# Kernel tuning notes

Measured on AMD Instinct MI355X. Metric: run time of the kernel, lower is better.

The kernel has to match this reference:

```python
import jax, jax.numpy as jnp
import numpy as np

BS, X_RW, H = 16384, 768, 256  # batch, x + R*W, hidden
D_IN = X_RW + 2 * H            # 1280 = x + R*W + 2*h


def setup_inputs() -> dict:
    key = jax.random.key(0)
    ks = jax.random.split(key, 13)
    scale = 1.0 / np.sqrt(D_IN)  # nn.Linear default init range
    def lin(kw, kb):
        w = jax.random.uniform(kw, (D_IN, H), jnp.float32, -scale, scale)
        b = jax.random.uniform(kb, (H,), jnp.float32, -scale, scale)
        return w, b
    Wi, bi = lin(ks[0], ks[1])
    Wf, bf = lin(ks[2], ks[3])
    Wo, bo = lin(ks[4], ks[5])
    Ws, bs_ = lin(ks[6], ks[7])
    return {
        "input_x": jax.random.normal(ks[8], (BS, X_RW), jnp.float32),
        "previous_time": jax.random.normal(ks[9], (BS, H), jnp.float32),
        "previous_layer": jax.random.normal(ks[10], (BS, H), jnp.float32),
        "old_state": jax.random.normal(ks[11], (BS, H), jnp.float32),
        "Wi": Wi, "bi": bi, "Wf": Wf, "bf": bf,
        "Wo": Wo, "bo": bo, "Ws": Ws, "bs_": bs_,
    }


def reference(input_x, previous_time, previous_layer, old_state,
              Wi, bi, Wf, bf, Wo, bo, Ws, bs_):
    # concat once, fuse the four gate GEMMs into one [D_IN, 4H] GEMM
    s = jnp.concatenate([input_x, previous_time, previous_layer], axis=1)  # [bs, D_IN]
    W4 = jnp.concatenate([Wi, Wf, Wo, Ws], axis=1)   # [D_IN, 4H]
    b4 = jnp.concatenate([bi, bf, bo, bs_], axis=0)  # [4H]
    g = s @ W4 + b4                                   # [bs, 4H]
    i_g, f_g, o_g, c_g = jnp.split(g, 4, axis=1)
    input_gate = jax.nn.sigmoid(i_g)
    forget_gate = jax.nn.sigmoid(f_g)
    output_gate = jax.nn.sigmoid(o_g)
    new_state = forget_gate * old_state + input_gate * jnp.tanh(c_g)
    new_hidden = output_gate * jnp.tanh(new_state)
    return (new_hidden, new_state)
```

## Files before the change

kernel.cpp:

```cpp
#include <hip/hip_runtime.h>
#include <stdint.h>

#define BS   16384
#define XRW  768
#define HD   256
#define DIN  1280
#define N4   1024
#define NKT  20

typedef __attribute__((ext_vector_type(4))) float f32x4;
typedef __attribute__((ext_vector_type(8))) short s16x8;
typedef __attribute__((ext_vector_type(4))) unsigned int u32x4;

__device__ __forceinline__ unsigned short f2bf(float f) {
  uint32_t u = __builtin_bit_cast(uint32_t, f);
  u += 0x7FFFu + ((u >> 16) & 1u);
  return (unsigned short)(u >> 16);
}
__device__ __forceinline__ uint32_t cvtpk(float a, float b) {
  uint32_t d;
  asm("v_cvt_pk_bf16_f32 %0, %1, %2" : "=v"(d) : "v"(a), "v"(b));
  return d;
}
__device__ __forceinline__ float sigmoidf_(float x) {
  return 1.0f / (1.0f + __expf(-x));
}
__device__ __forceinline__ float tanhf_(float x) {
  return 1.0f - 2.0f / (__expf(2.0f * x) + 1.0f);
}
__device__ __forceinline__ void gload16(const void* g, void* l) {
  __builtin_amdgcn_global_load_lds((const __attribute__((address_space(1))) void*)g,
                                   (__attribute__((address_space(3))) void*)l, 16, 0, 0);
}

__global__ void conv_w_kernel(const float* __restrict__ Wi,
                              const float* __restrict__ Wf,
                              const float* __restrict__ Wo,
                              const float* __restrict__ Ws,
                              unsigned short* __restrict__ Wt) {
  const int np = blockIdx.x;
  const int g = (np >> 4) & 3;
  const int h = ((np >> 6) << 4) + (np & 15);
  const float* W = (g == 0) ? Wi : (g == 1) ? Wf : (g == 2) ? Wo : Ws;
  for (int k = threadIdx.x; k < DIN; k += 256)
    Wt[np * DIN + k] = f2bf(W[k * HD + h]);
}

__global__ __launch_bounds__(512, 2)
void lstm_gemm_kernel(const float* __restrict__ X,
                      const float* __restrict__ PT,
                      const float* __restrict__ PL,
                      const unsigned short* __restrict__ Wt,
                      const float* __restrict__ BI,
                      const float* __restrict__ BF,
                      const float* __restrict__ BO,
                      const float* __restrict__ BSv,
                      const float* __restrict__ OLD,
                      float* __restrict__ out) {
  __shared__ unsigned char smem[131072];
  const int tid  = threadIdx.x;
  const int wid  = tid >> 6;
  const int lane = tid & 63;

  const int H = blockIdx.x;
  const int xcd = H & 7, slot = H >> 3;
  const int mt = xcd * 8 + (slot >> 2);
  const int nt = slot & 3;
  const int wr = wid >> 2, wc = wid & 3;

  const int r8   = lane >> 3;
  const int scol = ((lane & 7) ^ r8) << 4;
  const char* gB = (const char*)Wt + (size_t)(nt * 256 + wid * 8 + r8) * (DIN * 2) + scol;

#define STAGE_B(t1, oB) do {                                                  \
    const int kb_ = (t1) * 128;                                               \
    _Pragma("unroll")                                                         \
    for (int c_ = 0; c_ < 4; ++c_)                                            \
      gload16(gB + (size_t)c_ * (64 * DIN * 2) + kb_,                         \
              &smem[65536 + (oB) + c_ * 8192 + wid * 1024]);                  \
  } while (0)

  const int arow  = tid >> 3;
  const int a7    = tid & 7;
  const int awcol = ((a7 ^ (arow & 7)) << 4);

#define ALOAD(t1, h, R0, R1, R2, R3) do {                                     \
    const float* asrc_; int astr_, aoff_;                                     \
    if ((t1) < 12)      { asrc_ = X;  astr_ = XRW; aoff_ = (t1) * 64; }       \
    else if ((t1) < 16) { asrc_ = PT; astr_ = HD;  aoff_ = ((t1) - 12) * 64; }\
    else                { asrc_ = PL; astr_ = HD;  aoff_ = ((t1) - 16) * 64; }\
    const float* ga_ = asrc_ + (size_t)(mt * 256 + arow + (h) * 128) * astr_  \
                             + aoff_ + a7 * 8;                                \
    R0 = *(const f32x4*)(ga_);                                                \
    R1 = *(const f32x4*)(ga_ + 4);                                            \
    R2 = *(const f32x4*)(ga_ + (size_t)64 * astr_);                           \
    R3 = *(const f32x4*)(ga_ + (size_t)64 * astr_ + 4);                       \
  } while (0)

#define AWRITE(oB, h, R0, R1, R2, R3) do {                                    \
    u32x4 w0_, w1_;                                                           \
    w0_.x = cvtpk(R0.x, R0.y); w0_.y = cvtpk(R0.z, R0.w);                     \
    w0_.z = cvtpk(R1.x, R1.y); w0_.w = cvtpk(R1.z, R1.w);                     \
    w1_.x = cvtpk(R2.x, R2.y); w1_.y = cvtpk(R2.z, R2.w);                     \
    w1_.z = cvtpk(R3.x, R3.y); w1_.w = cvtpk(R3.z, R3.w);                     \
    *(u32x4*)(&smem[(oB) + ((arow + (h) * 128)      << 7) + awcol]) = w0_;    \
    *(u32x4*)(&smem[(oB) + ((arow + (h) * 128 + 64) << 7) + awcol]) = w1_;    \
  } while (0)

  const int rx   = lane & 15;
  const int axor = (lane & 7) << 4;
  const int col0 = (((lane >> 4) << 4)) ^ axor;
  const int col1 = (64 + ((lane >> 4) << 4)) ^ axor;
  const int aRow = (wr * 128 + rx) * 128;
  const int bRow = 65536 + (wc * 64 + rx) * 128;

  f32x4 acc[8][4];
  #pragma unroll
  for (int i = 0; i < 8; ++i)
    #pragma unroll
    for (int j = 0; j < 4; ++j) {
      f32x4 z = {0.0f, 0.0f, 0.0f, 0.0f};
      acc[i][j] = z;
    }

#define VMW(N) asm volatile("s_waitcnt vmcnt(" #N ")" ::: "memory")
#define LGKM0() do { asm volatile("s_waitcnt lgkmcnt(0)" ::: "memory");       \
                     __builtin_amdgcn_sched_barrier(0); } while (0)
#define FRAGS(bo_, kh_col) do {                                               \
    _Pragma("unroll")                                                         \
    for (int mf = 0; mf < 8; ++mf)                                            \
      aq[mf] = *(const s16x8*)(&smem[(bo_) + aRow + mf * 2048 + (kh_col)]);   \
    _Pragma("unroll")                                                         \
    for (int nf = 0; nf < 4; ++nf)                                            \
      bq[nf] = *(const s16x8*)(&smem[(bo_) + bRow + nf * 2048 + (kh_col)]);   \
  } while (0)
#define MFMAS() do {                                                          \
    __builtin_amdgcn_s_setprio(1);                                            \
    _Pragma("unroll")                                                         \
    for (int mf = 0; mf < 8; ++mf)                                            \
      _Pragma("unroll")                                                       \
      for (int nf = 0; nf < 4; ++nf)                                          \
        acc[mf][nf] = __builtin_amdgcn_mfma_f32_16x16x32_bf16(aq[mf], bq[nf], \
                                                      acc[mf][nf], 0, 0, 0);  \
    __builtin_amdgcn_s_setprio(0);                                            \
  } while (0)

  {
    f32x4 p0, p1, p2, p3;
    ALOAD(0, 0, p0, p1, p2, p3);
    STAGE_B(0, 0);
    VMW(4);
    AWRITE(0, 0, p0, p1, p2, p3);
    ALOAD(0, 1, p0, p1, p2, p3);
    VMW(0);
    AWRITE(0, 1, p0, p1, p2, p3);
    LGKM0();
    __builtin_amdgcn_s_barrier();
  }

  for (int kt = 0; kt < NKT; ++kt) {
    const int c = kt & 1, o = c ^ 1;
    const int bo_ = c << 15;
    const int oo_ = o << 15;
    const bool pf = (kt + 1) < NKT;
    s16x8 aq[8], bq[4];
    f32x4 ar0, ar1, ar2, ar3;

    if (pf) ALOAD(kt + 1, 0, ar0, ar1, ar2, ar3);
    FRAGS(bo_, col0);
    if (pf) STAGE_B(kt + 1, oo_);
    LGKM0();
    MFMAS();
    VMW(4);
    if (pf) { AWRITE(oo_, 0, ar0, ar1, ar2, ar3); ALOAD(kt + 1, 1, ar0, ar1, ar2, ar3); }
    FRAGS(bo_, col1);
    LGKM0();
    MFMAS();
    VMW(0);
    if (pf) AWRITE(oo_, 1, ar0, ar1, ar2, ar3);
    LGKM0();
    __builtin_amdgcn_s_barrier();
  }

  {
    const int hq = nt * 64 + wc * 16 + rx;
    const float bbi = BI[hq], bbf = BF[hq], bbo = BO[hq], bbs = BSv[hq];
    const int m0 = mt * 256 + wr * 128 + (lane >> 4) * 4;
    float* outNS = out + (size_t)BS * HD;
    #pragma unroll
    for (int mf = 0; mf < 8; ++mf) {
      const int mrow = m0 + mf * 16;
      float old_[4];
      #pragma unroll
      for (int r = 0; r < 4; ++r)
        old_[r] = OLD[(size_t)(mrow + r) * HD + hq];
      #pragma unroll
      for (int r = 0; r < 4; ++r) {
        const float ig = sigmoidf_(acc[mf][0][r] + bbi);
        const float fg = sigmoidf_(acc[mf][1][r] + bbf);
        const float og = sigmoidf_(acc[mf][2][r] + bbo);
        const float cg = tanhf_(acc[mf][3][r] + bbs);
        const float ns = fg * old_[r] + ig * cg;
        const float nh = og * tanhf_(ns);
        out[(size_t)(mrow + r) * HD + hq]   = nh;
        outNS[(size_t)(mrow + r) * HD + hq] = ns;
      }
    }
  }
#undef STAGE_B
#undef ALOAD
#undef AWRITE
#undef VMW
#undef LGKM0
#undef FRAGS
#undef MFMAS
}

extern "C" void kernel_launch(void* const* d_in, const int* in_sizes, int n_in,
                              void* d_out, int out_size, void* d_ws, size_t ws_size,
                              hipStream_t stream) {
  const float* X   = (const float*)d_in[0];
  const float* PT  = (const float*)d_in[1];
  const float* PL  = (const float*)d_in[2];
  const float* OLD = (const float*)d_in[3];
  const float* Wi  = (const float*)d_in[4];
  const float* bi  = (const float*)d_in[5];
  const float* Wf  = (const float*)d_in[6];
  const float* bfv = (const float*)d_in[7];
  const float* Wo  = (const float*)d_in[8];
  const float* bo  = (const float*)d_in[9];
  const float* Ws  = (const float*)d_in[10];
  const float* bsv = (const float*)d_in[11];
  float* out = (float*)d_out;

  unsigned short* Wt = (unsigned short*)d_ws;

  conv_w_kernel<<<N4, 256, 0, stream>>>(Wi, Wf, Wo, Ws, Wt);
  lstm_gemm_kernel<<<256, 512, 0, stream>>>(X, PT, PL, Wt, bi, bfv, bo, bsv, OLD, out);
}
```

Measured before the change: 63.12 us.

## Triple-buffer weight tiles and prefetch both A halves, one barrier per K-step

The weight (B) tiles in LDS go from double to triple buffering, so each tile is staged two K-steps ahead. Both halves of the next A tile are issued as global loads at the start of each step, instead of the second half waiting until mid-step. The K loop is unrolled by six with fixed buffer indices, leaving one s_waitcnt/barrier pair per step, to hide global load latency better behind the MFMAs. In exchange, LDS use rises to 160KB per block and register pressure grows from holding eight prefetched A vectors, which may limit occupancy or cause spills.

```diff
diff --git a/kernel.cpp b/kernel.cpp
--- a/kernel.cpp
+++ b/kernel.cpp
@@ -57,7 +57,7 @@
                       const float* __restrict__ BSv,
                       const float* __restrict__ OLD,
                       float* __restrict__ out) {
-  __shared__ unsigned char smem[131072];
+  __shared__ unsigned char smem[163840];
   const int tid  = threadIdx.x;
   const int wid  = tid >> 6;
   const int lane = tid & 63;
@@ -72,12 +72,12 @@
   const int scol = ((lane & 7) ^ r8) << 4;
   const char* gB = (const char*)Wt + (size_t)(nt * 256 + wid * 8 + r8) * (DIN * 2) + scol;
 
-#define STAGE_B(t1, oB) do {                                                  \
+#define STAGE_B(t1, BB) do {                                                  \
     const int kb_ = (t1) * 128;                                               \
     _Pragma("unroll")                                                         \
     for (int c_ = 0; c_ < 4; ++c_)                                            \
       gload16(gB + (size_t)c_ * (64 * DIN * 2) + kb_,                         \
-              &smem[65536 + (oB) + c_ * 8192 + wid * 1024]);                  \
+              &smem[65536 + (BB) * 32768 + c_ * 8192 + wid * 1024]);          \
   } while (0)
 
   const int arow  = tid >> 3;
@@ -97,14 +97,14 @@
     R3 = *(const f32x4*)(ga_ + (size_t)64 * astr_ + 4);                       \
   } while (0)
 
-#define AWRITE(oB, h, R0, R1, R2, R3) do {                                    \
+#define AWRITE(AB, h, R0, R1, R2, R3) do {                                    \
     u32x4 w0_, w1_;                                                           \
     w0_.x = cvtpk(R0.x, R0.y); w0_.y = cvtpk(R0.z, R0.w);                     \
     w0_.z = cvtpk(R1.x, R1.y); w0_.w = cvtpk(R1.z, R1.w);                     \
     w1_.x = cvtpk(R2.x, R2.y); w1_.y = cvtpk(R2.z, R2.w);                     \
     w1_.z = cvtpk(R3.x, R3.y); w1_.w = cvtpk(R3.z, R3.w);                     \
-    *(u32x4*)(&smem[(oB) + ((arow + (h) * 128)      << 7) + awcol]) = w0_;    \
-    *(u32x4*)(&smem[(oB) + ((arow + (h) * 128 + 64) << 7) + awcol]) = w1_;    \
+    *(u32x4*)(&smem[(AB) * 32768 + ((arow + (h) * 128)      << 7) + awcol]) = w0_; \
+    *(u32x4*)(&smem[(AB) * 32768 + ((arow + (h) * 128 + 64) << 7) + awcol]) = w1_; \
   } while (0)
 
   const int rx   = lane & 15;
@@ -112,7 +112,7 @@
   const int col0 = (((lane >> 4) << 4)) ^ axor;
   const int col1 = (64 + ((lane >> 4) << 4)) ^ axor;
   const int aRow = (wr * 128 + rx) * 128;
-  const int bRow = 65536 + (wc * 64 + rx) * 128;
+  const int bRow = (wc * 64 + rx) * 128;
 
   f32x4 acc[8][4];
   #pragma unroll
@@ -126,13 +126,13 @@
 #define VMW(N) asm volatile("s_waitcnt vmcnt(" #N ")" ::: "memory")
 #define LGKM0() do { asm volatile("s_waitcnt lgkmcnt(0)" ::: "memory");       \
                      __builtin_amdgcn_sched_barrier(0); } while (0)
-#define FRAGS(bo_, kh_col) do {                                               \
+#define FRAGS(AB, BB, kh_col) do {                                            \
     _Pragma("unroll")                                                         \
     for (int mf = 0; mf < 8; ++mf)                                            \
-      aq[mf] = *(const s16x8*)(&smem[(bo_) + aRow + mf * 2048 + (kh_col)]);   \
+      aq[mf] = *(const s16x8*)(&smem[(AB) * 32768 + aRow + mf * 2048 + (kh_col)]); \
     _Pragma("unroll")                                                         \
     for (int nf = 0; nf < 4; ++nf)                                            \
-      bq[nf] = *(const s16x8*)(&smem[(bo_) + bRow + nf * 2048 + (kh_col)]);   \
+      bq[nf] = *(const s16x8*)(&smem[65536 + (BB) * 32768 + bRow + nf * 2048 + (kh_col)]); \
   } while (0)
 #define MFMAS() do {                                                          \
     __builtin_amdgcn_s_setprio(1);                                            \
@@ -145,41 +145,70 @@
     __builtin_amdgcn_s_setprio(0);                                            \
   } while (0)
 
-  {
-    f32x4 p0, p1, p2, p3;
-    ALOAD(0, 0, p0, p1, p2, p3);
+#define TILE(t1, AR, BR, BW) do {                                             \
+    s16x8 aq[8], bq[4];                                                       \
+    f32x4 h00, h01, h02, h03, h10, h11, h12, h13;                             \
+    ALOAD((t1) + 1, 0, h00, h01, h02, h03);                                   \
+    ALOAD((t1) + 1, 1, h10, h11, h12, h13);                                   \
+    FRAGS(AR, BR, col0);                                                      \
+    STAGE_B((t1) + 2, BW);                                                    \
+    LGKM0();                                                                  \
+    MFMAS();                                                                  \
+    VMW(4);                                                                   \
+    AWRITE((AR) ^ 1, 0, h00, h01, h02, h03);                                  \
+    AWRITE((AR) ^ 1, 1, h10, h11, h12, h13);                                  \
+    FRAGS(AR, BR, col1);                                                      \
+    LGKM0();                                                                  \
+    MFMAS();                                                                  \
+    __builtin_amdgcn_s_barrier();                                             \
+  } while (0)
+
+  {
+    f32x4 h00, h01, h02, h03, h10, h11, h12, h13;
+    ALOAD(0, 0, h00, h01, h02, h03);
+    ALOAD(0, 1, h10, h11, h12, h13);
     STAGE_B(0, 0);
+    STAGE_B(1, 1);
+    VMW(8);
+    AWRITE(0, 0, h00, h01, h02, h03);
+    AWRITE(0, 1, h10, h11, h12, h13);
     VMW(4);
-    AWRITE(0, 0, p0, p1, p2, p3);
-    ALOAD(0, 1, p0, p1, p2, p3);
+    LGKM0();
+    __builtin_amdgcn_s_barrier();
+  }
+
+  for (int j = 0; j < 18; j += 6) {
+    TILE(j + 0, 0, 0, 2);
+    TILE(j + 1, 1, 1, 0);
+    TILE(j + 2, 0, 2, 1);
+    TILE(j + 3, 1, 0, 2);
+    TILE(j + 4, 0, 1, 0);
+    TILE(j + 5, 1, 2, 1);
+  }
+  {
+    s16x8 aq[8], bq[4];
+    f32x4 h00, h01, h02, h03, h10, h11, h12, h13;
+    ALOAD(19, 0, h00, h01, h02, h03);
+    ALOAD(19, 1, h10, h11, h12, h13);
+    FRAGS(0, 0, col0);
+    LGKM0();
+    MFMAS();
     VMW(0);
-    AWRITE(0, 1, p0, p1, p2, p3);
-    LGKM0();
+    AWRITE(1, 0, h00, h01, h02, h03);
+    AWRITE(1, 1, h10, h11, h12, h13);
+    FRAGS(0, 0, col1);
+    LGKM0();
+    MFMAS();
     __builtin_amdgcn_s_barrier();
   }
-
-  for (int kt = 0; kt < NKT; ++kt) {
-    const int c = kt & 1, o = c ^ 1;
-    const int bo_ = c << 15;
-    const int oo_ = o << 15;
-    const bool pf = (kt + 1) < NKT;
+  {
     s16x8 aq[8], bq[4];
-    f32x4 ar0, ar1, ar2, ar3;
-
-    if (pf) ALOAD(kt + 1, 0, ar0, ar1, ar2, ar3);
-    FRAGS(bo_, col0);
-    if (pf) STAGE_B(kt + 1, oo_);
-    LGKM0();
-    MFMAS();
-    VMW(4);
-    if (pf) { AWRITE(oo_, 0, ar0, ar1, ar2, ar3); ALOAD(kt + 1, 1, ar0, ar1, ar2, ar3); }
-    FRAGS(bo_, col1);
-    LGKM0();
-    MFMAS();
-    VMW(0);
-    if (pf) AWRITE(oo_, 1, ar0, ar1, ar2, ar3);
-    LGKM0();
-    __builtin_amdgcn_s_barrier();
+    FRAGS(1, 1, col0);
+    LGKM0();
+    MFMAS();
+    FRAGS(1, 1, col1);
+    LGKM0();
+    MFMAS();
   }
 
   {
@@ -214,6 +243,7 @@
 #undef LGKM0
 #undef FRAGS
 #undef MFMAS
+#undef TILE
 }
 
 extern "C" void kernel_launch(void* const* d_in, const int* in_sizes, int n_in,
```

Measured after the change: 81.97 us. 29.9% more time.
